# Kernel optimization log

Hardware: AMD Instinct MI355X
Metric: run time of the kernel (lower is better)

The kernel has to match this reference:

```python
import jax, jax.numpy as jnp
import numpy as np

B, N, E = 2, 2048, 2048
H, D = 16, 128
BASE = 10000.0


def rope(t, offset=0):
    # t: [b, n, h, d] -- rotary position embedding (Lrpe type 1), half-rotation form
    d = t.shape[-1]
    pos = jnp.arange(t.shape[1], dtype=jnp.float32) + offset
    inv = BASE ** (-jnp.arange(0, d, 2, dtype=jnp.float32) / d)  # [d/2]
    ang = pos[:, None] * inv[None, :]                            # [n, d/2]
    cos = jnp.cos(ang)[None, :, None, :]
    sin = jnp.sin(ang)[None, :, None, :]
    t1, t2 = t[..., : d // 2], t[..., d // 2 :]
    return jnp.concatenate([t1 * cos - t2 * sin, t2 * cos + t1 * sin], axis=-1)


def setup_inputs() -> dict:
    key = jax.random.key(0)
    ks = jax.random.split(key, 6)
    s = lambda k, shape, fan: jax.random.normal(k, shape, jnp.float32) / np.sqrt(fan)
    return {
        "x": jax.random.normal(ks[0], (B, N, E), jnp.float32),
        "Wq": s(ks[1], (H * D, E), E),      # q_proj.weight
        "Wkv": s(ks[2], (2 * D, E), E),     # kv_proj.weight
        "Wkvh": s(ks[3], (2 * H, E), E),    # kv_head_proj.weight
        "Wg": s(ks[4], (2 * H, E), E),      # gate_proj.weight (gate_type=1)
        "Wout": s(ks[5], (E, H * D), H * D) # out_proj.weight
    }


def reference(x, Wq, Wkv, Wkvh, Wg, Wout):
    b, n, _ = x.shape
    q = (x @ Wq.T).reshape(b, n, H, D)
    kv = x @ Wkv.T            # [b, n, 2D]
    kv_head = x @ Wkvh.T      # [b, n, 2H] (mpa_type=0, activation 'none')

    # gate_type == 1: log-sigmoid gated cumulative-sum decay on kv_head (GLA-style)
    g = x @ Wg.T                                                       # [b, n, 2H]
    log_f = jnp.concatenate(
        [jnp.zeros((b, 1, 2 * H), jnp.float32), jax.nn.log_sigmoid(g)], axis=1
    )
    log_f_cumsum = jnp.cumsum(log_f, axis=1)[:, :-1]                   # [b, n, 2H]
    kv_head = kv_head * jnp.exp(log_f_cumsum)
    kv_head = jnp.cumsum(kv_head, axis=1)

    kp, vp = kv[..., :D], kv[..., D:]
    kh, vh = kv_head[..., :H], kv_head[..., H:]
    # low-rank KV expansion: outer product of shared (d) with per-head scalar (h)
    k = jnp.einsum('bnd,bnh->bnhd', kp, kh)
    v = jnp.einsum('bnd,bnh->bnhd', vp, vh)

    q = rope(q)
    k = rope(k)

    # causal softmax attention (flash_attn_func equivalent), scale = D**-0.5
    scale = 1.0 / np.sqrt(D)
    scores = jnp.einsum('bnhd,bmhd->bhnm', q, k) * scale
    mask = jnp.tril(jnp.ones((n, n), bool))
    scores = jnp.where(mask[None, None], scores, -jnp.inf)
    p = jax.nn.softmax(scores, axis=-1)
    o = jnp.einsum('bhnm,bmhd->bnhd', p, v).reshape(b, n, H * D)
    return o @ Wout.T
```

## Files before the change

kernel.cpp:

```cpp
#include <hip/hip_runtime.h>
#include <hip/hip_bf16.h>
#include <math.h>

typedef __attribute__((ext_vector_type(8))) short bf16x8;
typedef __attribute__((ext_vector_type(4))) float f32x4;

#define MFMA16(a, b, c) __builtin_amdgcn_mfma_f32_16x16x32_bf16((a), (b), (c), 0, 0, 0)

static __device__ __forceinline__ float fast_exp2(float x) { return __builtin_amdgcn_exp2f(x); }

static __device__ __forceinline__ unsigned short f2bf(float f) {
  __hip_bfloat16 h = __float2bfloat16(f);
  unsigned short u;
  __builtin_memcpy(&u, &h, 2);
  return u;
}
static __device__ __forceinline__ float bf2f(unsigned short u) {
  unsigned int x = ((unsigned int)u) << 16;
  float f;
  __builtin_memcpy(&f, &x, 4);
  return f;
}

static __device__ __forceinline__ void cast8(const float* __restrict__ src,
                                             unsigned short* __restrict__ dst, int blk, int tid) {
  int i = (blk * 256 + tid) * 8;
  float4 a = *(const float4*)(src + i);
  float4 b = *(const float4*)(src + i + 4);
  union { unsigned short u[8]; bf16x8 v; } o;
  o.u[0] = f2bf(a.x); o.u[1] = f2bf(a.y); o.u[2] = f2bf(a.z); o.u[3] = f2bf(a.w);
  o.u[4] = f2bf(b.x); o.u[5] = f2bf(b.y); o.u[6] = f2bf(b.z); o.u[7] = f2bf(b.w);
  *(bf16x8*)(dst + i) = o.v;
}

__global__ __launch_bounds__(256) void prep(const float* __restrict__ x, const float* __restrict__ Wq,
                                            const float* __restrict__ Wout, const float* __restrict__ Wkv,
                                            const float* __restrict__ Wkvh, const float* __restrict__ Wg,
                                            unsigned short* __restrict__ x_bf, unsigned short* __restrict__ wq_bf,
                                            unsigned short* __restrict__ wout_bf, unsigned short* __restrict__ wsm_bf,
                                            float2* __restrict__ cs, float* __restrict__ wgt) {
  int bid = blockIdx.x, tid = threadIdx.x;
  if (bid < 4096) {
    cast8(x, x_bf, bid, tid);
  } else if (bid < 6144) {
    cast8(Wq, wq_bf, bid - 4096, tid);
  } else if (bid < 8192) {
    cast8(Wout, wout_bf, bid - 6144, tid);
  } else if (bid < 8576) {
    int row = bid - 8192;
    int c = tid * 8;
    const float* src = nullptr;
    if (row < 256) src = Wkv + (size_t)row * 2048;
    else if (row < 288) src = Wkvh + (size_t)(row - 256) * 2048;
    union { unsigned short u[8]; bf16x8 v; } o;
    if (src) {
      float4 a = *(const float4*)(src + c);
      float4 b = *(const float4*)(src + c + 4);
      o.u[0] = f2bf(a.x); o.u[1] = f2bf(a.y); o.u[2] = f2bf(a.z); o.u[3] = f2bf(a.w);
      o.u[4] = f2bf(b.x); o.u[5] = f2bf(b.y); o.u[6] = f2bf(b.z); o.u[7] = f2bf(b.w);
    } else {
      for (int j = 0; j < 8; j++) o.u[j] = 0;
    }
    *(bf16x8*)(wsm_bf + (size_t)row * 2048 + c) = o.v;
  } else if (bid < 9088) {
    int i = (bid - 8576) * 256 + tid;
    int f = i & 63, n = i >> 6;
    float inv = powf(10000.0f, -(float)(2 * f) / 128.0f);
    float ang = (float)n * inv;
    cs[i] = make_float2(cosf(ang), sinf(ang));
  } else {
    int i = (bid - 9088) * 256 + tid;
    int oc = i >> 11, k = i & 2047;
    wgt[(size_t)k * 32 + oc] = Wg[i];
  }
}

__global__ __launch_bounds__(256) void gproj(const float* __restrict__ x, const float* __restrict__ Wgt,
                                             float* __restrict__ lsg_t) {
  int tid = blockIdx.x * 256 + threadIdx.x;
  int tok = tid >> 5, oc = tid & 31;
  const float* xr = x + (size_t)tok * 2048;
  float acc = 0.f;
  for (int k = 0; k < 2048; k += 4) {
    float4 a = *(const float4*)(xr + k);
    acc += a.x * Wgt[(size_t)k * 32 + oc] + a.y * Wgt[(size_t)(k + 1) * 32 + oc] +
           a.z * Wgt[(size_t)(k + 2) * 32 + oc] + a.w * Wgt[(size_t)(k + 3) * 32 + oc];
  }
  float ls = (acc >= 0.f) ? -log1pf(expf(-acc)) : acc - log1pf(expf(acc));
  int b = tok >> 11, n = tok & 2047;
  lsg_t[((size_t)(b * 32 + oc)) * 2048 + n] = ls;
}

template <int MODE>
static __device__ __forceinline__ void gemm_body(const unsigned short* __restrict__ A,
                                                 const unsigned short* __restrict__ B,
                                                 float* __restrict__ Cf,
                                                 unsigned short* __restrict__ Cb,
                                                 int K, int ldc, int lin, int nbx, int cpx) {
  __shared__ unsigned short As[128 * 64];
  __shared__ unsigned short Bs[128 * 64];
  int tid = threadIdx.x;
  int wave = tid >> 6, lane = tid & 63, l15 = lane & 15, lg = lane >> 4;
  int wr = wave >> 1, wc = wave & 1;
  int swz = (lin & 7) * cpx + (lin >> 3);
  int bx = swz % nbx, by = swz / nbx;
  int row0 = by * 128, col0 = bx * 128;
  int rsw = l15 & 7;
  f32x4 acc[4][4];
#pragma unroll
  for (int m = 0; m < 4; m++)
#pragma unroll
    for (int n = 0; n < 4; n++) acc[m][n] = (f32x4){0.f, 0.f, 0.f, 0.f};

  for (int k0 = 0; k0 < K; k0 += 64) {
#pragma unroll
    for (int c = 0; c < 4; c++) {
      int chunk = c * 256 + tid;
      int r = chunk >> 3, sl = chunk & 7;
      int kk = (sl ^ (r & 7)) * 8;
      __builtin_amdgcn_global_load_lds(
          (const __attribute__((address_space(1))) void*)(A + (size_t)(row0 + r) * K + k0 + kk),
          (__attribute__((address_space(3))) void*)(As + ((size_t)c * 256 + wave * 64) * 8), 16, 0, 0);
      __builtin_amdgcn_global_load_lds(
          (const __attribute__((address_space(1))) void*)(B + (size_t)(col0 + r) * K + k0 + kk),
          (__attribute__((address_space(3))) void*)(Bs + ((size_t)c * 256 + wave * 64) * 8), 16, 0, 0);
    }
    __syncthreads();
    bf16x8 af[4][2], bfr[4][2];
#pragma unroll
    for (int m = 0; m < 4; m++)
#pragma unroll
      for (int ks = 0; ks < 2; ks++)
        af[m][ks] = *(const bf16x8*)&As[(wr * 64 + m * 16 + l15) * 64 + ((ks * 4 + lg) ^ rsw) * 8];
#pragma unroll
    for (int n = 0; n < 4; n++)
#pragma unroll
      for (int ks = 0; ks < 2; ks++)
        bfr[n][ks] = *(const bf16x8*)&Bs[(wc * 64 + n * 16 + l15) * 64 + ((ks * 4 + lg) ^ rsw) * 8];
#pragma unroll
    for (int ks = 0; ks < 2; ks++)
#pragma unroll
      for (int m = 0; m < 4; m++)
#pragma unroll
        for (int n = 0; n < 4; n++) acc[m][n] = MFMA16(af[m][ks], bfr[n][ks], acc[m][n]);
    __syncthreads();
  }

  if (MODE == 0 || col0 >= 2048) {
#pragma unroll
    for (int m = 0; m < 4; m++) {
      int row_b = row0 + wr * 64 + m * 16 + lg * 4;
#pragma unroll
      for (int n = 0; n < 4; n++) {
        int col = col0 + wc * 64 + n * 16 + l15;
        int cw = (MODE == 0) ? col : (col - 2048);
#pragma unroll
        for (int j = 0; j < 4; j++) {
          Cf[(size_t)(row_b + j) * ldc + cw] = acc[m][n][j];
        }
      }
    }
  } else {
#pragma unroll
    for (int m = 0; m < 4; m++) {
      int row_b = row0 + wr * 64 + m * 16 + lg * 4;
#pragma unroll
      for (int n = 0; n < 4; n++) {
        int col = col0 + wc * 64 + n * 16 + l15;
        int h = col >> 7, d = col & 127;
#pragma unroll
        for (int j = 0; j < 4; j++) {
          int row = row_b + j;
          int b = row >> 11, nn = row & 2047;
          Cb[(((size_t)b * 16 + h) * 2048 + nn) * 128 + d] = f2bf(acc[m][n][j]);
        }
      }
    }
  }
}

__global__ __launch_bounds__(256) void gemm_q(const unsigned short* __restrict__ A,
                                              const unsigned short* __restrict__ B,
                                              float* __restrict__ small_out,
                                              unsigned short* __restrict__ q_r) {
  gemm_body<1>(A, B, small_out, q_r, 2048, 384, (int)(blockIdx.y * 19 + blockIdx.x), 19, 76);
}

__global__ __launch_bounds__(256) void gemm_out(const unsigned short* __restrict__ A,
                                                const unsigned short* __restrict__ B,
                                                float* __restrict__ C) {
  gemm_body<0>(A, B, C, nullptr, 2048, 2048, (int)(blockIdx.y * 16 + blockIdx.x), 16, 64);
}

__global__ __launch_bounds__(256) void scan_kernel(const float* __restrict__ lsg_t,
                                                   const float* __restrict__ so,
                                                   float* __restrict__ khvh) {
  int b = blockIdx.x >> 5, ch = blockIdx.x & 31;
  int t = threadIdx.x, lane = t & 63, wv = t >> 6;
  const float* L = lsg_t + ((size_t)(b * 32 + ch)) * 2048 + t * 8;
  float ls[8], v[8];
  float4 a = *(const float4*)L, c = *(const float4*)(L + 4);
  ls[0] = a.x; ls[1] = a.y; ls[2] = a.z; ls[3] = a.w;
  ls[4] = c.x; ls[5] = c.y; ls[6] = c.z; ls[7] = c.w;
  const float* V = so + ((size_t)(b * 2048 + t * 8)) * 384 + 256 + ch;
#pragma unroll
  for (int j = 0; j < 8; j++) v[j] = V[(size_t)j * 384];
  float run = 0.f;
#pragma unroll
  for (int j = 0; j < 8; j++) run += ls[j];
  float incl = run;
#pragma unroll
  for (int off = 1; off < 64; off <<= 1) {
    float nv = __shfl_up(incl, off);
    if (lane >= off) incl += nv;
  }
  __shared__ float ws[2][4];
  if (lane == 63) ws[0][wv] = incl;
  __syncthreads();
  float wbase = 0.f;
#pragma unroll
  for (int w = 0; w < 4; w++) wbase += (w < wv) ? ws[0][w] : 0.f;
  float baseA = wbase + incl - run;
  float lf = baseA, s = 0.f;
#pragma unroll
  for (int j = 0; j < 8; j++) { s += v[j] * __expf(lf); lf += ls[j]; }
  float incl2 = s;
#pragma unroll
  for (int off = 1; off < 64; off <<= 1) {
    float nv = __shfl_up(incl2, off);
    if (lane >= off) incl2 += nv;
  }
  if (lane == 63) ws[1][wv] = incl2;
  __syncthreads();
  float wbase2 = 0.f;
#pragma unroll
  for (int w = 0; w < 4; w++) wbase2 += (w < wv) ? ws[1][w] : 0.f;
  float base2 = wbase2 + incl2 - s;
  lf = baseA; s = base2;
  float* O = khvh + ((size_t)(b * 2048 + t * 8)) * 32 + ch;
#pragma unroll
  for (int j = 0; j < 8; j++) { s += v[j] * __expf(lf); lf += ls[j]; O[(size_t)j * 32] = s; }
}

__global__ __launch_bounds__(256) void build_kv2(const float* __restrict__ so,
                                                 const float* __restrict__ khvh,
                                                 const float2* __restrict__ cs,
                                                 unsigned short* __restrict__ k_r,
                                                 unsigned short* __restrict__ v_t) {
  int ntb = blockIdx.x, bh = blockIdx.y;
  int b = bh >> 4, h = bh & 15;
  int tok0 = b * 2048 + ntb * 64;
  int n0 = ntb * 64;
  __shared__ float khs[64], vhs[64];
  __shared__ unsigned short Vt_s[64 * 132];
  int t = threadIdx.x;
  if (t < 64) {
    khs[t] = khvh[(size_t)(tok0 + t) * 32 + h];
    vhs[t] = khvh[(size_t)(tok0 + t) * 32 + 16 + h];
  }
  __syncthreads();
#pragma unroll
  for (int c = 0; c < 4; c++) {
    int idx = c * 256 + t;
    int r = idx >> 4, q4 = (idx & 15) * 4;
    const float* sop = so + (size_t)(tok0 + r) * 384;
    float4 k1 = *(const float4*)(sop + q4);
    float4 k2 = *(const float4*)(sop + 64 + q4);
    float kh = khs[r];
    int n = n0 + r;
    union { unsigned short u[4]; uint2 v2; } o1, o2;
#pragma unroll
    for (int j = 0; j < 4; j++) {
      float2 cc = cs[(n << 6) + q4 + j];
      float av = ((const float*)&k1)[j], bv = ((const float*)&k2)[j];
      o1.u[j] = f2bf((av * cc.x - bv * cc.y) * kh);
      o2.u[j] = f2bf((bv * cc.x + av * cc.y) * kh);
    }
    size_t off = ((size_t)bh * 2048 + n) * 128 + q4;
    *(uint2*)(k_r + off) = o1.v2;
    *(uint2*)(k_r + off + 64) = o2.v2;
  }
#pragma unroll
  for (int c = 0; c < 8; c++) {
    int idx = c * 256 + t;
    int r = idx >> 5, d4 = (idx & 31) * 4;
    const float* sop = so + (size_t)(tok0 + r) * 384 + 128;
    float4 v = *(const float4*)(sop + d4);
    float vh = vhs[r];
    union { unsigned short u[4]; uint2 v2; } ov;
#pragma unroll
    for (int j = 0; j < 4; j++) ov.u[j] = f2bf(((const float*)&v)[j] * vh);
    *(uint2*)&Vt_s[r * 132 + d4] = ov.v2;
  }
  __syncthreads();
#pragma unroll
  for (int c = 0; c < 4; c++) {
    int idx = c * 256 + t;
    int d = idx >> 3, c8 = (idx & 7) * 8;
    union { unsigned short u[8]; bf16x8 v; } o;
#pragma unroll
    for (int j = 0; j < 8; j++) o.u[j] = Vt_s[(c8 + j) * 132 + d];
    *(bf16x8*)(v_t + ((size_t)bh * 128 + d) * 2048 + n0 + c8) = o.v;
  }
}

__global__ __launch_bounds__(256, 2) void flash_attn(const unsigned short* __restrict__ q_r,
                                                     const unsigned short* __restrict__ k_r,
                                                     const unsigned short* __restrict__ v_t,
                                                     const float2* __restrict__ cs,
                                                     unsigned short* __restrict__ o) {
  int lin = blockIdx.y * 16 + blockIdx.x;
  int swz = (lin & 7) * 64 + (lin >> 3);
  int bx = swz & 15, bh = swz >> 4;
  const unsigned short* Kg = k_r + (size_t)bh * 2048 * 128;
  const unsigned short* Vtg = v_t + (size_t)bh * 128 * 2048;
  __shared__ unsigned short Ks[2][64 * 128];
  __shared__ unsigned short VTs[2][128 * 64];
  __shared__ unsigned short Ps[4][16 * 72];
  int tid = threadIdx.x, wave = tid >> 6, lane = tid & 63, l15 = lane & 15, lg = lane >> 4;
  int sw = (l15 & 7) * 8;
  int b = bh >> 4, h = bh & 15;

  union { unsigned short u[8]; bf16x8 v; } onesu;
#pragma unroll
  for (int j = 0; j < 8; j++) onesu.u[j] = 0x3F80;
  const bf16x8 ones = onesu.v;

  int qtA = bx, qtB = 31 - bx;
  int qt = qtA;

  bf16x8 qf[4];
#define LOAD_Q()                                                                                   \
  {                                                                                                \
    const unsigned short* Qg = q_r + ((size_t)bh * 2048 + qt * 64) * 128;                          \
    int n = qt * 64 + wave * 16 + l15;                                                             \
    union { unsigned short u[8]; bf16x8 v; } r0, r1, r2, r3;                                       \
    r0.v = *(const bf16x8*)(Qg + (wave * 16 + l15) * 128 + 0 * 32 + lg * 8);                       \
    r1.v = *(const bf16x8*)(Qg + (wave * 16 + l15) * 128 + 1 * 32 + lg * 8);                       \
    r2.v = *(const bf16x8*)(Qg + (wave * 16 + l15) * 128 + 2 * 32 + lg * 8);                       \
    r3.v = *(const bf16x8*)(Qg + (wave * 16 + l15) * 128 + 3 * 32 + lg * 8);                       \
    union { unsigned short u[8]; bf16x8 v; } o0, o1, o2, o3;                                       \
    _Pragma("unroll") for (int j = 0; j < 8; j++) {                                                \
      float2 c0 = cs[(n << 6) + 0 * 32 + lg * 8 + j];                                              \
      float t1 = bf2f(r0.u[j]), t2 = bf2f(r2.u[j]);                                                \
      o0.u[j] = f2bf(t1 * c0.x - t2 * c0.y);                                                       \
      o2.u[j] = f2bf(t2 * c0.x + t1 * c0.y);                                                       \
      float2 c1 = cs[(n << 6) + 1 * 32 + lg * 8 + j];                                              \
      float s1 = bf2f(r1.u[j]), s2 = bf2f(r3.u[j]);                                                \
      o1.u[j] = f2bf(s1 * c1.x - s2 * c1.y);                                                       \
      o3.u[j] = f2bf(s2 * c1.x + s1 * c1.y);                                                       \
    }                                                                                              \
    qf[0] = o0.v; qf[1] = o1.v; qf[2] = o2.v; qf[3] = o3.v;                                        \
  }

  LOAD_Q();

  float m_r[4], l_r[4];
  f32x4 oacc[8];
#pragma unroll
  for (int j = 0; j < 4; j++) { m_r[j] = -INFINITY; l_r[j] = 0.f; }
#pragma unroll
  for (int db = 0; db < 8; db++) oacc[db] = (f32x4){0.f, 0.f, 0.f, 0.f};

  const float kscale = 0.12753102f;
  const float THR = 11.0f;

#define STAGE(kt, bsel)                                                                           \
  {                                                                                               \
    int kti = (kt);                                                                               \
    int bs = (bsel);                                                                              \
    _Pragma("unroll") for (int c = 0; c < 4; c++) {                                               \
      int s = c * 256 + tid;                                                                      \
      int kr = s >> 4, kc = ((s & 15) ^ (kr & 7)) * 8;                                            \
      __builtin_amdgcn_global_load_lds(                                                           \
          (const __attribute__((address_space(1))) void*)(Kg + (size_t)(kti * 64 + kr) * 128 + kc),\
          (__attribute__((address_space(3))) void*)(&Ks[bs][(c * 256 + wave * 64) * 8]), 16, 0, 0);\
      int vr = s >> 3, vc = ((s & 7) ^ (vr & 7)) * 8;                                             \
      __builtin_amdgcn_global_load_lds(                                                           \
          (const __attribute__((address_space(1))) void*)(Vtg + (size_t)vr * 2048 + kti * 64 + vc),\
          (__attribute__((address_space(3))) void*)(&VTs[bs][(c * 256 + wave * 64) * 8]), 16, 0, 0);\
    }                                                                                             \
  }

  STAGE(0, 0);
  __syncthreads();

  for (int s = 0; s < 33; ++s) {
    int nb = s & 1;
    if (s + 1 < 33) {
      int nk = (s + 1 <= qtA) ? (s + 1) : (s + 1 - (qtA + 1));
      STAGE(nk, nb ^ 1);
    }
    int kt = (s <= qtA) ? s : (s - (qtA + 1));
    bool diag = (s == qtA) || (s == 32);
    int qrow0 = qt * 64 + wave * 16 + lg * 4;

    f32x4 sc[4];
#pragma unroll
    for (int cb = 0; cb < 4; cb++) sc[cb] = (f32x4){0.f, 0.f, 0.f, 0.f};
    __builtin_amdgcn_s_setprio(1);
#pragma unroll
    for (int kk = 0; kk < 4; kk++) {
#pragma unroll
      for (int cb = 0; cb < 4; cb++) {
        bf16x8 kf = *(const bf16x8*)&Ks[nb][(cb * 16 + l15) * 128 + ((kk * 32 + lg * 8) ^ sw)];
        sc[cb] = MFMA16(qf[kk], kf, sc[cb]);
      }
    }
    __builtin_amdgcn_s_setprio(0);
    if (diag) {
#pragma unroll
      for (int cb = 0; cb < 4; cb++) {
        int col = kt * 64 + cb * 16 + l15;
#pragma unroll
        for (int j = 0; j < 4; j++) {
          float v = sc[cb][j] * kscale;
          if (col > qrow0 + j) v = -INFINITY;
          sc[cb][j] = v;
        }
      }
    } else {
#pragma unroll
      for (int cb = 0; cb < 4; cb++)
#pragma unroll
        for (int j = 0; j < 4; j++) sc[cb][j] *= kscale;
    }
    float pm[4];
#pragma unroll
    for (int j = 0; j < 4; j++)
      pm[j] = fmaxf(fmaxf(sc[0][j], sc[1][j]), fmaxf(sc[2][j], sc[3][j]));
    bool grow = !__all((pm[0] <= m_r[0] + THR) & (pm[1] <= m_r[1] + THR) &
                       (pm[2] <= m_r[2] + THR) & (pm[3] <= m_r[3] + THR));
    if (grow) {
#pragma unroll
      for (int off = 1; off < 16; off <<= 1) {
#pragma unroll
        for (int j = 0; j < 4; j++) pm[j] = fmaxf(pm[j], __shfl_xor(pm[j], off));
      }
#pragma unroll
      for (int j = 0; j < 4; j++) {
        float mn = fmaxf(m_r[j], pm[j]);
        float corr = fast_exp2(m_r[j] - mn);
        m_r[j] = mn;
        l_r[j] *= corr;
#pragma unroll
        for (int db = 0; db < 8; db++) oacc[db][j] *= corr;
      }
    }
#pragma unroll
    for (int cb = 0; cb < 4; cb++)
#pragma unroll
      for (int j = 0; j < 4; j++)
        Ps[wave][(lg * 4 + j) * 72 + cb * 16 + l15] = f2bf(fast_exp2(sc[cb][j] - m_r[j]));
    f32x4 sacc = (f32x4){0.f, 0.f, 0.f, 0.f};
    __builtin_amdgcn_s_setprio(1);
#pragma unroll
    for (int kc = 0; kc < 2; kc++) {
      bf16x8 pa = *(const bf16x8*)&Ps[wave][l15 * 72 + kc * 32 + lg * 8];
      sacc = MFMA16(pa, ones, sacc);
#pragma unroll
      for (int db = 0; db < 8; db++) {
        bf16x8 vb = *(const bf16x8*)&VTs[nb][(db * 16 + l15) * 64 + ((kc * 32 + lg * 8) ^ sw)];
        oacc[db] = MFMA16(pa, vb, oacc[db]);
      }
    }
    __builtin_amdgcn_s_setprio(0);
#pragma unroll
    for (int j = 0; j < 4; j++) l_r[j] += sacc[j];
    __syncthreads();

    if (s == qtA) {
      int qrow_e = qt * 64 + wave * 16 + lg * 4;
#pragma unroll
      for (int db = 0; db < 8; db++) {
        int d = db * 16 + l15;
#pragma unroll
        for (int j = 0; j < 4; j++) {
          float val = oacc[db][j] / l_r[j];
          o[((size_t)(b * 2048 + qrow_e + j)) * 2048 + h * 128 + d] = f2bf(val);
        }
      }
      qt = qtB;
      LOAD_Q();
#pragma unroll
      for (int j = 0; j < 4; j++) { m_r[j] = -INFINITY; l_r[j] = 0.f; }
#pragma unroll
      for (int db = 0; db < 8; db++) oacc[db] = (f32x4){0.f, 0.f, 0.f, 0.f};
    }
  }
  int qrow_e = qt * 64 + wave * 16 + lg * 4;
#pragma unroll
  for (int db = 0; db < 8; db++) {
    int d = db * 16 + l15;
#pragma unroll
    for (int j = 0; j < 4; j++) {
      float val = oacc[db][j] / l_r[j];
      o[((size_t)(b * 2048 + qrow_e + j)) * 2048 + h * 128 + d] = f2bf(val);
    }
  }
#undef STAGE
#undef LOAD_Q
}

extern "C" void kernel_launch(void* const* d_in, const int* in_sizes, int n_in,
                              void* d_out, int out_size, void* d_ws, size_t ws_size,
                              hipStream_t stream) {
  (void)in_sizes; (void)n_in; (void)out_size; (void)ws_size;
  const float* x    = (const float*)d_in[0];
  const float* Wq   = (const float*)d_in[1];
  const float* Wkv  = (const float*)d_in[2];
  const float* Wkvh = (const float*)d_in[3];
  const float* Wg   = (const float*)d_in[4];
  const float* Wout = (const float*)d_in[5];
  float* out = (float*)d_out;

  char* ws = (char*)d_ws;
  size_t off = 0;
  auto alloc = [&](size_t bytes) -> void* {
    void* p = ws + off;
    off += (bytes + 255) & ~(size_t)255;
    return p;
  };
  unsigned short* x_bf    = (unsigned short*)alloc(4096ull * 2048 * 2);
  unsigned short* wq_bf   = (unsigned short*)alloc(2048ull * 2048 * 2);
  unsigned short* wsm_bf  = (unsigned short*)alloc(384ull * 2048 * 2);
  unsigned short* wout_bf = (unsigned short*)alloc(2048ull * 2048 * 2);
  unsigned short* q_r     = (unsigned short*)alloc(4096ull * 2048 * 2);
  unsigned short* k_r     = (unsigned short*)alloc(4096ull * 2048 * 2);
  unsigned short* o_bf    = (unsigned short*)alloc(4096ull * 2048 * 2);
  float* small_out        = (float*)alloc(4096ull * 384 * 4);
  float* lsg_t            = (float*)alloc(64ull * 2048 * 4);
  float* khvh             = (float*)alloc(4096ull * 32 * 4);
  float2* cs              = (float2*)alloc(2048ull * 64 * 8);
  float* wgt              = (float*)alloc(2048ull * 32 * 4);
  unsigned short* v_t     = x_bf;

  prep<<<9344, 256, 0, stream>>>(x, Wq, Wout, Wkv, Wkvh, Wg, x_bf, wq_bf, wout_bf, wsm_bf, cs, wgt);
  gproj<<<512, 256, 0, stream>>>(x, wgt, lsg_t);
  gemm_q<<<dim3(19, 32), 256, 0, stream>>>(x_bf, wq_bf, small_out, q_r);
  scan_kernel<<<64, 256, 0, stream>>>(lsg_t, small_out, khvh);
  build_kv2<<<dim3(32, 32), 256, 0, stream>>>(small_out, khvh, cs, k_r, v_t);
  flash_attn<<<dim3(16, 32), 256, 0, stream>>>(q_r, k_r, v_t, cs, o_bf);
  gemm_out<<<dim3(16, 32), 256, 0, stream>>>(o_bf, wout_bf, out);
}
```

Before: 282.4 us.

## Load V directly to registers, fold softmax scale into Q, drop GEMM LDS swizzle

```diff
diff --git a/kernel.cpp b/kernel.cpp
--- a/kernel.cpp
+++ b/kernel.cpp
@@ -105,7 +105,6 @@
   int swz = (lin & 7) * cpx + (lin >> 3);
   int bx = swz % nbx, by = swz / nbx;
   int row0 = by * 128, col0 = bx * 128;
-  int rsw = l15 & 7;
   f32x4 acc[4][4];
 #pragma unroll
   for (int m = 0; m < 4; m++)
@@ -116,8 +115,7 @@
 #pragma unroll
     for (int c = 0; c < 4; c++) {
       int chunk = c * 256 + tid;
-      int r = chunk >> 3, sl = chunk & 7;
-      int kk = (sl ^ (r & 7)) * 8;
+      int r = chunk >> 3, kk = (chunk & 7) * 8;
       __builtin_amdgcn_global_load_lds(
           (const __attribute__((address_space(1))) void*)(A + (size_t)(row0 + r) * K + k0 + kk),
           (__attribute__((address_space(3))) void*)(As + ((size_t)c * 256 + wave * 64) * 8), 16, 0, 0);
@@ -131,12 +129,12 @@
     for (int m = 0; m < 4; m++)
 #pragma unroll
       for (int ks = 0; ks < 2; ks++)
-        af[m][ks] = *(const bf16x8*)&As[(wr * 64 + m * 16 + l15) * 64 + ((ks * 4 + lg) ^ rsw) * 8];
+        af[m][ks] = *(const bf16x8*)&As[(wr * 64 + m * 16 + l15) * 64 + ks * 32 + lg * 8];
 #pragma unroll
     for (int n = 0; n < 4; n++)
 #pragma unroll
       for (int ks = 0; ks < 2; ks++)
-        bfr[n][ks] = *(const bf16x8*)&Bs[(wc * 64 + n * 16 + l15) * 64 + ((ks * 4 + lg) ^ rsw) * 8];
+        bfr[n][ks] = *(const bf16x8*)&Bs[(wc * 64 + n * 16 + l15) * 64 + ks * 32 + lg * 8];
 #pragma unroll
     for (int ks = 0; ks < 2; ks++)
 #pragma unroll
@@ -304,7 +302,7 @@
   }
 }
 
-__global__ __launch_bounds__(256, 2) void flash_attn(const unsigned short* __restrict__ q_r,
+__global__ __launch_bounds__(256, 3) void flash_attn(const unsigned short* __restrict__ q_r,
                                                      const unsigned short* __restrict__ k_r,
                                                      const unsigned short* __restrict__ v_t,
                                                      const float2* __restrict__ cs,
@@ -315,7 +313,6 @@
   const unsigned short* Kg = k_r + (size_t)bh * 2048 * 128;
   const unsigned short* Vtg = v_t + (size_t)bh * 128 * 2048;
   __shared__ unsigned short Ks[2][64 * 128];
-  __shared__ unsigned short VTs[2][128 * 64];
   __shared__ unsigned short Ps[4][16 * 72];
   int tid = threadIdx.x, wave = tid >> 6, lane = tid & 63, l15 = lane & 15, lg = lane >> 4;
   int sw = (l15 & 7) * 8;
@@ -328,6 +325,9 @@
 
   int qtA = bx, qtB = 31 - bx;
   int qt = qtA;
+
+  const float kscale = 0.12753102f;
+  const float THR = 11.0f;
 
   bf16x8 qf[4];
 #define LOAD_Q()                                                                                   \
@@ -343,12 +343,12 @@
     _Pragma("unroll") for (int j = 0; j < 8; j++) {                                                \
       float2 c0 = cs[(n << 6) + 0 * 32 + lg * 8 + j];                                              \
       float t1 = bf2f(r0.u[j]), t2 = bf2f(r2.u[j]);                                                \
-      o0.u[j] = f2bf(t1 * c0.x - t2 * c0.y);                                                       \
-      o2.u[j] = f2bf(t2 * c0.x + t1 * c0.y);                                                       \
+      o0.u[j] = f2bf((t1 * c0.x - t2 * c0.y) * kscale);                                            \
+      o2.u[j] = f2bf((t2 * c0.x + t1 * c0.y) * kscale);                                            \
       float2 c1 = cs[(n << 6) + 1 * 32 + lg * 8 + j];                                              \
       float s1 = bf2f(r1.u[j]), s2 = bf2f(r3.u[j]);                                                \
-      o1.u[j] = f2bf(s1 * c1.x - s2 * c1.y);                                                       \
-      o3.u[j] = f2bf(s2 * c1.x + s1 * c1.y);                                                       \
+      o1.u[j] = f2bf((s1 * c1.x - s2 * c1.y) * kscale);                                            \
+      o3.u[j] = f2bf((s2 * c1.x + s1 * c1.y) * kscale);                                            \
     }                                                                                              \
     qf[0] = o0.v; qf[1] = o1.v; qf[2] = o2.v; qf[3] = o3.v;                                        \
   }
@@ -361,9 +361,6 @@
   for (int j = 0; j < 4; j++) { m_r[j] = -INFINITY; l_r[j] = 0.f; }
 #pragma unroll
   for (int db = 0; db < 8; db++) oacc[db] = (f32x4){0.f, 0.f, 0.f, 0.f};
-
-  const float kscale = 0.12753102f;
-  const float THR = 11.0f;
 
 #define STAGE(kt, bsel)                                                                           \
   {                                                                                               \
@@ -375,10 +372,6 @@
       __builtin_amdgcn_global_load_lds(                                                           \
           (const __attribute__((address_space(1))) void*)(Kg + (size_t)(kti * 64 + kr) * 128 + kc),\
           (__attribute__((address_space(3))) void*)(&Ks[bs][(c * 256 + wave * 64) * 8]), 16, 0, 0);\
-      int vr = s >> 3, vc = ((s & 7) ^ (vr & 7)) * 8;                                             \
-      __builtin_amdgcn_global_load_lds(                                                           \
-          (const __attribute__((address_space(1))) void*)(Vtg + (size_t)vr * 2048 + kti * 64 + vc),\
-          (__attribute__((address_space(3))) void*)(&VTs[bs][(c * 256 + wave * 64) * 8]), 16, 0, 0);\
     }                                                                                             \
   }
 
@@ -395,6 +388,14 @@
     bool diag = (s == qtA) || (s == 32);
     int qrow0 = qt * 64 + wave * 16 + lg * 4;
 
+    bf16x8 vb[2][8];
+#pragma unroll
+    for (int kc = 0; kc < 2; kc++)
+#pragma unroll
+      for (int db = 0; db < 8; db++)
+        vb[kc][db] = *(const bf16x8*)(Vtg + (size_t)(db * 16 + l15) * 2048 +
+                                      kt * 64 + kc * 32 + lg * 8);
+
     f32x4 sc[4];
 #pragma unroll
     for (int cb = 0; cb < 4; cb++) sc[cb] = (f32x4){0.f, 0.f, 0.f, 0.f};
@@ -414,16 +415,9 @@
         int col = kt * 64 + cb * 16 + l15;
 #pragma unroll
         for (int j = 0; j < 4; j++) {
-          float v = sc[cb][j] * kscale;
-          if (col > qrow0 + j) v = -INFINITY;
-          sc[cb][j] = v;
+          if (col > qrow0 + j) sc[cb][j] = -INFINITY;
         }
       }
-    } else {
-#pragma unroll
-      for (int cb = 0; cb < 4; cb++)
-#pragma unroll
-        for (int j = 0; j < 4; j++) sc[cb][j] *= kscale;
     }
     float pm[4];
 #pragma unroll
@@ -460,8 +454,7 @@
       sacc = MFMA16(pa, ones, sacc);
 #pragma unroll
       for (int db = 0; db < 8; db++) {
-        bf16x8 vb = *(const bf16x8*)&VTs[nb][(db * 16 + l15) * 64 + ((kc * 32 + lg * 8) ^ sw)];
-        oacc[db] = MFMA16(pa, vb, oacc[db]);
+        oacc[db] = MFMA16(pa, vb[kc][db], oacc[db]);
       }
     }
     __builtin_amdgcn_s_setprio(0);
```

Result: slower. 426.2 us (+50.9%).
